# Kernel tuning notes

Measured on AMD Instinct MI355X. Metric: run time of the kernel, lower is better.

## Reference

```python
import jax, jax.numpy as jnp
import numpy as np
from jax import lax

B, L, E, P, K, KS, H, T = 64, 512, 256, 64, 512, 3, 512, 53
V, MAXL = 50000, 512


def _span_idx(k):
    ks, kl = jax.random.split(k)
    starts = jax.random.randint(ks, (B,), 1, L - 9)
    spans = jax.random.randint(kl, (B,), 0, 8)
    return jnp.stack([starts, starts + spans], axis=1)  # [B,2], 1<=s<=e<L-1


def setup_inputs() -> dict:
    key = jax.random.key(0)
    ks = jax.random.split(key, 12)
    context = jax.random.randint(ks[0], (B, L), 0, V)
    subject_idx = _span_idx(ks[1])
    object_idx = _span_idx(ks[2])
    subject_dis = jax.random.randint(ks[3], (B, L), 0, 2 * MAXL)
    object_dis = jax.random.randint(ks[4], (B, L), 0, 2 * MAXL)
    embed_table = jax.random.normal(ks[5], (V, E), jnp.float32) * 0.02
    pos_table = jax.random.normal(ks[6], (2 * MAXL, P), jnp.float32) * 0.02
    Cin = 3 * E + 2 * P
    conv_w = jax.random.normal(ks[7], (K, Cin, KS), jnp.float32) * 0.02
    conv_b = jnp.zeros((K,), jnp.float32)
    lin1_w = jax.random.normal(ks[8], (H, K), jnp.float32) * 0.02
    lin1_b = jnp.zeros((H,), jnp.float32)
    lin2_w = jax.random.normal(ks[9], (T, 6 * E + H), jnp.float32) * 0.02
    lin2_b = jnp.zeros((T,), jnp.float32)
    return {"context": context, "subject_idx": subject_idx, "object_idx": object_idx,
            "subject_dis": subject_dis, "object_dis": object_dis,
            "embed_table": embed_table, "pos_table": pos_table,
            "conv_w": conv_w, "conv_b": conv_b,
            "lin1_w": lin1_w, "lin1_b": lin1_b, "lin2_w": lin2_w, "lin2_b": lin2_b}


def _entity_features(embed, idx):
    # embed: [B,L,E'], idx: [B,2] (start,end) inclusive span
    s, e = idx[:, 0], idx[:, 1]
    pos = jnp.arange(L)
    mask = (pos[None, :] >= s[:, None]) & (pos[None, :] <= e[:, None])  # [B,L]
    cnt = mask.sum(axis=1).astype(embed.dtype)[:, None]
    mean = jnp.einsum('ble,bl->be', embed, mask.astype(embed.dtype)) / cnt
    bidx = jnp.arange(embed.shape[0])
    left = embed[bidx, s - 1]                       # start>=1 always in data (torch: start>=0 branch)
    right_ok = (e + 1) < L
    right = jnp.where(right_ok[:, None], embed[bidx, jnp.clip(e + 1, 0, L - 1)], 0.0)
    return jnp.concatenate([mean, left, right], axis=1)  # [B,3E']


def reference(context, subject_idx, object_idx, subject_dis, object_dis,
              embed_table, pos_table, conv_w, conv_b,
              lin1_w, lin1_b, lin2_w, lin2_b):
    embed = embed_table[context]                    # [B,L,E]
    subj = _entity_features(embed, subject_idx)     # [B,3E]
    obj = _entity_features(embed, object_idx)       # [B,3E]

    # shift-and-concat window features (zero pad one step each side)
    epad = jnp.pad(embed, ((0, 0), (1, 1), (0, 0)))
    word = jnp.concatenate([epad[:, :-2], epad[:, 1:-1], epad[:, 2:]], axis=2)  # [B,L,3E]

    pos_feat = jnp.concatenate([pos_table[subject_dis], pos_table[object_dis]], axis=2)  # [B,L,2P]
    sent = jnp.concatenate([word, pos_feat], axis=2).transpose(0, 2, 1)  # [B,C,L]

    conv = lax.conv_general_dilated(sent, conv_w, window_strides=(1,),
                                    padding=[(KS // 2, KS // 2)],
                                    dimension_numbers=('NCH', 'OIH', 'NCH'))
    conv = conv + conv_b[None, :, None]             # [B,K,L]
    pooled = conv.max(axis=2)                       # global maxpool -> [B,K]
    sent_h = jnp.tanh(pooled @ lin1_w.T + lin1_b)   # [B,H]

    com = jnp.concatenate([subj, obj, sent_h], axis=1)  # [B,6E+H]
    scores = com @ lin2_w.T + lin2_b                # [B,T]; decode = argmax(scores, 1)
    return scores
```

## Files before the change

### kernel.cpp

```cpp
#include <hip/hip_runtime.h>
#include <hip/hip_bf16.h>
#include <hip/hip_fp8.h>
#include <stdint.h>

#define B_   64
#define L_   512
#define E_   256
#define P_   64
#define KOUT 512
#define KS_  3
#define H_   512
#define T_   53
#define CINW 2688
#define LE   516
#define LPP  514
#define COMW 2048

#define FP8_S    64.0f
#define DESCALE  (1.0f / 4096.0f)

#define SEC_CW    0
#define SEC_EMBP  512
#define SEC_POSP  (SEC_EMBP + (B_ * LE / 4))
#define SEC_ENT   (SEC_POSP + (B_ * LPP / 4))
#define SEC_POOL  (SEC_ENT + 2 * B_)
#define SEC_END   (SEC_POOL + 32)

typedef __attribute__((ext_vector_type(4))) float f32x4;
typedef __attribute__((ext_vector_type(4))) int   i32x4;
typedef __attribute__((ext_vector_type(8))) int   i32x8;

__device__ __forceinline__ unsigned enc_f(float x) {
    unsigned u = __float_as_uint(x);
    return (u & 0x80000000u) ? ~u : (u | 0x80000000u);
}
__device__ __forceinline__ float dec_f(unsigned e) {
    return __uint_as_float((e & 0x80000000u) ? (e & 0x7fffffffu) : ~e);
}
__device__ __forceinline__ unsigned char f8c(float x) {
    __hip_fp8_e4m3 t(x);
    return t.__x;
}

__device__ __forceinline__ void cp16(const void* g, void* l) {
    __builtin_amdgcn_global_load_lds(
        (const __attribute__((address_space(1))) unsigned int*)g,
        (__attribute__((address_space(3))) unsigned int*)l,
        16, 0, 0);
}

__global__ void prep(const float* __restrict__ conv_w,
                     const int* __restrict__ context,
                     const int* __restrict__ sidx,
                     const int* __restrict__ oidx,
                     const int* __restrict__ sdis,
                     const int* __restrict__ odis,
                     const float* __restrict__ etab,
                     const float* __restrict__ ptab,
                     unsigned char* __restrict__ wce,
                     unsigned char* __restrict__ wcp,
                     unsigned char* __restrict__ embp,
                     unsigned char* __restrict__ posp,
                     float* __restrict__ corr,
                     float* __restrict__ com,
                     unsigned* __restrict__ pooled) {
    __shared__ float w[CINW];
    const int blk = blockIdx.x;
    const int tid = threadIdx.x;

    if (blk < SEC_EMBP) {
        int n = blk;
        const float* src = conv_w + (size_t)n * CINW;
        for (int i = tid; i < CINW; i += 256) w[i] = src[i];
        __syncthreads();
        for (int i = tid; i < 5 * E_; i += 256) {
            int d = i >> 8, c = i & 255;
            float s = 0.f;
#pragma unroll
            for (int tau = 0; tau <= 2; tau++) {
                int seg = d - tau;
                if (seg >= 0 && seg <= 2) s += w[(seg * 256 + c) * 3 + tau];
            }
            wce[((size_t)d * KOUT + n) * E_ + c] = f8c(s * FP8_S);
        }
        for (int i = tid; i < 3 * 128; i += 256) {
            int tau = i >> 7, p = i & 127;
            wcp[((size_t)tau * KOUT + n) * 128 + p] = f8c(w[(768 + p) * 3 + tau] * FP8_S);
        }
        {
            int p   = tid >> 1, sub = tid & 1;
            int bb  = p >> 1, which = p & 1;
            int token = context[bb * L_ + (which ? L_ - 1 : 0)];
            const float4* er4 = (const float4*)(etab + (size_t)token * E_ + sub * 128);
            int A = which ? (sub * 384 + 2) : (1536 + sub * 384);
            float s = 0.f;
#pragma unroll 8
            for (int c4 = 0; c4 < 32; c4++) {
                float4 v = er4[c4];
                int c = c4 * 4;
                s += v.x * w[A + 3 * c]     + v.y * w[A + 3 * c + 3]
                   + v.z * w[A + 3 * c + 6] + v.w * w[A + 3 * c + 9];
            }
            s += __shfl_xor(s, 1, 64);
            if (sub == 0) corr[(bb * 2 + which) * KOUT + n] = s;
        }
    } else if (blk < SEC_POSP) {
        int row = (blk - SEC_EMBP) * 4 + (tid >> 6);
        int lane = tid & 63;
        int b = row / LE, r = row % LE;
        unsigned char* out = embp + (size_t)row * E_;
        if (r < 2 || r >= LE - 2) {
            *(uchar4*)(out + lane * 4) = (uchar4){0, 0, 0, 0};
            return;
        }
        int token = context[b * L_ + (r - 2)];
        float4 v = *(const float4*)(etab + (size_t)token * E_ + lane * 4);
        uchar4 pk;
        pk.x = f8c(v.x * FP8_S); pk.y = f8c(v.y * FP8_S);
        pk.z = f8c(v.z * FP8_S); pk.w = f8c(v.w * FP8_S);
        *(uchar4*)(out + lane * 4) = pk;
    } else if (blk < SEC_ENT) {
        int row = (blk - SEC_POSP) * 4 + (tid >> 6);
        int lane = tid & 63;
        int b = row / LPP, r = row % LPP;
        unsigned char* out = posp + (size_t)row * 128;
        if (r < 1 || r >= LPP - 1) {
            *(unsigned short*)(out + lane * 2) = 0;
            return;
        }
        int l = r - 1;
        int which = lane >> 5;
        int i2 = (lane & 31) * 2;
        int t = which ? odis[b * L_ + l] : sdis[b * L_ + l];
        float2 v = *(const float2*)(ptab + (size_t)t * P_ + i2);
        unsigned short pk = (unsigned short)f8c(v.x * FP8_S)
                          | ((unsigned short)f8c(v.y * FP8_S) << 8);
        *(unsigned short*)(out + which * 64 + i2) = pk;
    } else if (blk < SEC_POOL) {
        int idx = blk - SEC_ENT;
        int b = idx >> 1, which = idx & 1;
        const int* sp = which ? oidx : sidx;
        int s = sp[b * 2 + 0], e = sp[b * 2 + 1];
        const int* ctx = context + b * L_;
        float* outb = com + (size_t)b * COMW + which * 768;
        int d = tid;
        float sum = 0.f;
        for (int x = s; x <= e; ++x) sum += etab[(size_t)ctx[x] * E_ + d];
        outb[d] = sum / (float)(e - s + 1);
        outb[256 + d] = etab[(size_t)ctx[s - 1] * E_ + d];
        float r = 0.f;
        if (e + 1 < L_) r = etab[(size_t)ctx[e + 1] * E_ + d];
        outb[512 + d] = r;
    } else {
        int base = ((blk - SEC_POOL) * 256 + tid) * 4;
        *(uint4*)(pooled + base) = (uint4){0, 0, 0, 0};
    }
}

__global__ void __launch_bounds__(256, 2)
conv_gemm_pool(const unsigned char* __restrict__ embp,
               const unsigned char* __restrict__ posp,
               const unsigned char* __restrict__ wce,
               const unsigned char* __restrict__ wcp,
               const float* __restrict__ corr,
               unsigned* __restrict__ pooled) {
    __shared__ unsigned char sT[2][2][128 * 128];

    const int tid  = threadIdx.x;
    const int lane = tid & 63;
    const int wave = tid >> 6;
    const int mt = blockIdx.x;
    const int nt = blockIdx.y;
    const int b  = mt >> 2;
    const int l0 = (mt & 3) * 128;
    const int n0 = nt * 128;

    const int wr = (wave & 1) * 64;
    const int wc = (wave >> 1) * 64;
    const int m  = lane & 15;
    const int q  = lane >> 4;

    f32x4 acc[4][4];
#pragma unroll
    for (int i = 0; i < 4; i++)
#pragma unroll
        for (int j = 0; j < 4; j++) acc[i][j] = (f32x4){0.f, 0.f, 0.f, 0.f};

    const int srow = tid >> 3;
    const int ssw  = ((tid & 7) ^ (srow & 7)) << 4;

    auto bases = [&](int t, const char*& A, int& As, const char*& Bx, int& Bs) {
        if (t < 10) {
            int tap = t >> 1, kc = (t & 1) << 7;
            A  = (const char*)embp + ((size_t)(b * LE + l0 + tap) << 8) + kc;
            As = E_;
            Bx = (const char*)wce + ((size_t)(tap * KOUT + n0) << 8) + kc;
            Bs = E_;
        } else {
            int tap = t - 10;
            A  = (const char*)posp + ((size_t)(b * LPP + l0 + tap) << 7);
            As = 128;
            Bx = (const char*)wcp + ((size_t)(tap * KOUT + n0) << 7);
            Bs = 128;
        }
    };

    auto stage = [&](int bf_, const char* A, int As, const char* Bx, int Bs) {
        char* dA = (char*)&sT[bf_][0][0] + tid * 16;
        char* dB = (char*)&sT[bf_][1][0] + tid * 16;
#pragma unroll
        for (int rnd = 0; rnd < 4; rnd++) {
            int r = srow + rnd * 32;
            cp16(A  + r * As + ssw, dA + rnd * 4096);
            cp16(Bx + r * Bs + ssw, dB + rnd * 4096);
        }
    };

    auto frag = [&](const unsigned char* base, int row) -> i32x8 {
        const unsigned char* rp = base + row * 128;
        int x  = (row & 7) << 4;
        i32x4 lo = *(const i32x4*)(rp + (((q << 1) << 4) ^ x));
        i32x4 hi = *(const i32x4*)(rp + ((((q << 1) | 1) << 4) ^ x));
        return (i32x8){lo[0], lo[1], lo[2], lo[3], hi[0], hi[1], hi[2], hi[3]};
    };

    auto compute = [&](int bf_) {
        const unsigned char* pA = &sT[bf_][0][0];
        const unsigned char* pB = &sT[bf_][1][0];
        i32x8 af[4];
#pragma unroll
        for (int i = 0; i < 4; i++) af[i] = frag(pA, wr + i * 16 + m);
#pragma unroll
        for (int j = 0; j < 4; j++) {
            i32x8 bfv = frag(pB, wc + j * 16 + m);
#pragma unroll
            for (int i = 0; i < 4; i++)
                acc[i][j] = __builtin_amdgcn_mfma_scale_f32_16x16x128_f8f6f4(
                    af[i], bfv, acc[i][j], 0, 0, 0, 0x7f7f7f7f, 0, 0x7f7f7f7f);
        }
    };

    {
        const char *A0, *B0; int As0, Bs0;
        bases(0, A0, As0, B0, Bs0);
        stage(0, A0, As0, B0, Bs0);
    }
    int cur = 0;
#pragma unroll 1
    for (int t = 0; t < 13; t++) {
        if (t < 12) {
            const char *A1, *B1; int As1, Bs1;
            bases(t + 1, A1, As1, B1, Bs1);
            stage(cur ^ 1, A1, As1, B1, Bs1);
            asm volatile("s_waitcnt vmcnt(8)" ::: "memory");
        } else {
            asm volatile("s_waitcnt vmcnt(0)" ::: "memory");
        }
        __builtin_amdgcn_s_barrier();
        __builtin_amdgcn_sched_barrier(0);
        compute(cur);
        __builtin_amdgcn_sched_barrier(0);
        __builtin_amdgcn_s_barrier();
        cur ^= 1;
    }

    const float* corrb = corr + b * 2 * KOUT;
#pragma unroll
    for (int j = 0; j < 4; j++) {
        int col = n0 + wc + j * 16 + m;
        float mx = -3.4e38f;
#pragma unroll
        for (int i = 0; i < 4; i++)
#pragma unroll
            for (int r = 0; r < 4; r++) {
                float v = acc[i][j][r] * DESCALE;
                int l = l0 + wr + i * 16 + q * 4 + r;
                if (l == 0)      v -= corrb[col];
                if (l == L_ - 1) v -= corrb[KOUT + col];
                mx = fmaxf(mx, v);
            }
        mx = fmaxf(mx, __shfl_xor(mx, 16, 64));
        mx = fmaxf(mx, __shfl_xor(mx, 32, 64));
        if (q == 0) atomicMax(&pooled[b * KOUT + col], enc_f(mx));
    }
}

__global__ void lin_fused(const unsigned* __restrict__ pooled,
                          const float* __restrict__ conv_b,
                          const float* __restrict__ lin1_w,
                          const float* __restrict__ lin1_b,
                          const float* __restrict__ com,
                          const float* __restrict__ lin2_w,
                          const float* __restrict__ lin2_b,
                          float* __restrict__ out) {
    __shared__ float padj[KOUT];
    __shared__ float sh[H_];
    const int b    = blockIdx.x;
    const int tid  = threadIdx.x;
    const int wave = tid >> 6, lane = tid & 63;

    if (tid < KOUT) padj[tid] = dec_f(pooled[b * KOUT + tid]) + conv_b[tid];
    __syncthreads();

#pragma unroll 1
    for (int hh = 0; hh < 32; ++hh) {
        int h = wave * 32 + hh;
        const float* w = lin1_w + (size_t)h * KOUT;
        float s = 0.f;
#pragma unroll
        for (int i = 0; i < 8; i++) {
            int k = lane + 64 * i;
            s += padj[k] * w[k];
        }
#pragma unroll
        for (int off = 32; off > 0; off >>= 1) s += __shfl_down(s, off, 64);
        if (lane == 0) sh[h] = tanhf(s + lin1_b[h]);
    }
    __syncthreads();

    const float* c = com + (size_t)b * COMW;
#pragma unroll 1
    for (int t = wave; t < T_; t += 16) {
        const float* w = lin2_w + (size_t)t * COMW;
        float s = 0.f;
#pragma unroll
        for (int i = 0; i < 24; i++) {
            int j = lane + 64 * i;
            s += c[j] * w[j];
        }
#pragma unroll
        for (int i = 24; i < 32; i++) {
            int j = lane + 64 * i;
            s += sh[j - 1536] * w[j];
        }
#pragma unroll
        for (int off = 32; off > 0; off >>= 1) s += __shfl_down(s, off, 64);
        if (lane == 0) out[b * T_ + t] = s + lin2_b[t];
    }
}

extern "C" void kernel_launch(void* const* d_in, const int* in_sizes, int n_in,
                              void* d_out, int out_size, void* d_ws, size_t ws_size,
                              hipStream_t stream) {
    const int*   context = (const int*)d_in[0];
    const int*   sidx    = (const int*)d_in[1];
    const int*   oidx    = (const int*)d_in[2];
    const int*   sdis    = (const int*)d_in[3];
    const int*   odis    = (const int*)d_in[4];
    const float* etab    = (const float*)d_in[5];
    const float* ptab    = (const float*)d_in[6];
    const float* conv_w  = (const float*)d_in[7];
    const float* conv_b  = (const float*)d_in[8];
    const float* lin1_w  = (const float*)d_in[9];
    const float* lin1_b  = (const float*)d_in[10];
    const float* lin2_w  = (const float*)d_in[11];
    const float* lin2_b  = (const float*)d_in[12];
    float* out = (float*)d_out;

    char* ws = (char*)d_ws;
    size_t off = 0;
    unsigned char* embp = (unsigned char*)(ws + off);
    off += (size_t)B_ * LE * E_;
    off = (off + 255) & ~(size_t)255;
    unsigned char* posp = (unsigned char*)(ws + off);
    off += (size_t)B_ * LPP * 128;
    off = (off + 255) & ~(size_t)255;
    unsigned char* wce = (unsigned char*)(ws + off);
    off += (size_t)5 * KOUT * E_;
    off = (off + 255) & ~(size_t)255;
    unsigned char* wcp = (unsigned char*)(ws + off);
    off += (size_t)3 * KOUT * 128;
    off = (off + 255) & ~(size_t)255;
    float* corr = (float*)(ws + off);
    off += (size_t)B_ * 2 * KOUT * 4;
    off = (off + 255) & ~(size_t)255;
    unsigned* pooled = (unsigned*)(ws + off);
    off += (size_t)B_ * KOUT * 4;
    off = (off + 255) & ~(size_t)255;
    float* com = (float*)(ws + off);
    off += (size_t)B_ * COMW * 4;

    prep<<<dim3(SEC_END), dim3(256), 0, stream>>>(
        conv_w, context, sidx, oidx, sdis, odis, etab, ptab,
        wce, wcp, embp, posp, corr, com, pooled);
    conv_gemm_pool<<<dim3(256, 4), dim3(256), 0, stream>>>(embp, posp, wce, wcp, corr, pooled);
    lin_fused<<<dim3(B_), dim3(1024), 0, stream>>>(
        pooled, conv_b, lin1_w, lin1_b, com, lin2_w, lin2_b, out);
}
```

Before: 190.3 us.

## Split fused linear tail into two highly parallel kernels

The single per-batch lin_fused kernel (64 blocks) is replaced by lin1_k, which computes each hidden unit in its own wave across 8192 blocks and writes the tanh output into the com buffer, and lin2_k, which computes each output score per wave over a 64x14 grid. This spreads the dense layers over all compute units instead of 64 blocks running long serial loops. It adds an extra kernel launch, a global round trip for the hidden activations, and redundant decoding of the pooled values per wave.

```diff
diff --git a/kernel.cpp b/kernel.cpp
--- a/kernel.cpp
+++ b/kernel.cpp
@@ -285,58 +285,47 @@
     }
 }
 
-__global__ void lin_fused(const unsigned* __restrict__ pooled,
-                          const float* __restrict__ conv_b,
-                          const float* __restrict__ lin1_w,
-                          const float* __restrict__ lin1_b,
-                          const float* __restrict__ com,
-                          const float* __restrict__ lin2_w,
-                          const float* __restrict__ lin2_b,
-                          float* __restrict__ out) {
-    __shared__ float padj[KOUT];
-    __shared__ float sh[H_];
-    const int b    = blockIdx.x;
-    const int tid  = threadIdx.x;
-    const int wave = tid >> 6, lane = tid & 63;
-
-    if (tid < KOUT) padj[tid] = dec_f(pooled[b * KOUT + tid]) + conv_b[tid];
-    __syncthreads();
-
-#pragma unroll 1
-    for (int hh = 0; hh < 32; ++hh) {
-        int h = wave * 32 + hh;
-        const float* w = lin1_w + (size_t)h * KOUT;
-        float s = 0.f;
-#pragma unroll
-        for (int i = 0; i < 8; i++) {
-            int k = lane + 64 * i;
-            s += padj[k] * w[k];
-        }
-#pragma unroll
-        for (int off = 32; off > 0; off >>= 1) s += __shfl_down(s, off, 64);
-        if (lane == 0) sh[h] = tanhf(s + lin1_b[h]);
-    }
-    __syncthreads();
-
+__global__ void lin1_k(const unsigned* __restrict__ pooled,
+                       const float* __restrict__ conv_b,
+                       const float* __restrict__ lin1_w,
+                       const float* __restrict__ lin1_b,
+                       float* __restrict__ com) {
+    int bid = blockIdx.x;
+    int wave = threadIdx.x >> 6, lane = threadIdx.x & 63;
+    int b = bid >> 7;
+    int h = (bid & 127) * 4 + wave;
+    const float* w = lin1_w + (size_t)h * KOUT;
+    const unsigned* pb = pooled + b * KOUT;
+    float s = 0.f;
+#pragma unroll
+    for (int i = 0; i < 8; i++) {
+        int k = lane + 64 * i;
+        s += (dec_f(pb[k]) + conv_b[k]) * w[k];
+    }
+#pragma unroll
+    for (int off = 32; off > 0; off >>= 1) s += __shfl_down(s, off, 64);
+    if (lane == 0) com[(size_t)b * COMW + 1536 + h] = tanhf(s + lin1_b[h]);
+}
+
+__global__ void lin2_k(const float* __restrict__ com,
+                       const float* __restrict__ lin2_w,
+                       const float* __restrict__ lin2_b,
+                       float* __restrict__ out) {
+    int b = blockIdx.x;
+    int wave = threadIdx.x >> 6, lane = threadIdx.x & 63;
+    int t = blockIdx.y * 4 + wave;
+    if (t >= T_) return;
+    const float* w = lin2_w + (size_t)t * COMW;
     const float* c = com + (size_t)b * COMW;
-#pragma unroll 1
-    for (int t = wave; t < T_; t += 16) {
-        const float* w = lin2_w + (size_t)t * COMW;
-        float s = 0.f;
-#pragma unroll
-        for (int i = 0; i < 24; i++) {
-            int j = lane + 64 * i;
-            s += c[j] * w[j];
-        }
-#pragma unroll
-        for (int i = 24; i < 32; i++) {
-            int j = lane + 64 * i;
-            s += sh[j - 1536] * w[j];
-        }
-#pragma unroll
-        for (int off = 32; off > 0; off >>= 1) s += __shfl_down(s, off, 64);
-        if (lane == 0) out[b * T_ + t] = s + lin2_b[t];
-    }
+    float s = 0.f;
+#pragma unroll
+    for (int i = 0; i < 32; i++) {
+        int k = lane + 64 * i;
+        s += c[k] * w[k];
+    }
+#pragma unroll
+    for (int off = 32; off > 0; off >>= 1) s += __shfl_down(s, off, 64);
+    if (lane == 0) out[b * T_ + t] = s + lin2_b[t];
 }
 
 extern "C" void kernel_launch(void* const* d_in, const int* in_sizes, int n_in,
@@ -384,6 +373,6 @@
         conv_w, context, sidx, oidx, sdis, odis, etab, ptab,
         wce, wcp, embp, posp, corr, com, pooled);
     conv_gemm_pool<<<dim3(256, 4), dim3(256), 0, stream>>>(embp, posp, wce, wcp, corr, pooled);
-    lin_fused<<<dim3(B_), dim3(1024), 0, stream>>>(
-        pooled, conv_b, lin1_w, lin1_b, com, lin2_w, lin2_b, out);
-}
+    lin1_k<<<dim3(8192), dim3(256), 0, stream>>>(pooled, conv_b, lin1_w, lin1_b, com);
+    lin2_k<<<dim3(B_, 14), dim3(256), 0, stream>>>(com, lin2_w, lin2_b, out);
+}
```

Result: faster. 178.9 us (-6.0%).
